# Kernel optimization log

Hardware: AMD Instinct MI355X
Metric: run time of the kernel (lower is better)

The kernel has to match this reference:

```python
import jax, jax.numpy as jnp
import numpy as np

B, D, H = 131072, 8, 128


def setup_inputs() -> dict:
    key = jax.random.key(0)
    ks = jax.random.split(key, 8)
    s1 = 1.0 / np.sqrt(D + 1)
    s2 = 1.0 / np.sqrt(H)
    return {
        "z": jax.random.normal(ks[0], (B, D), dtype=jnp.float32),
        "logp_z": jnp.zeros((B, 1), dtype=jnp.float32),
        "t": jax.random.uniform(ks[1], (1,), dtype=jnp.float32),
        "W1": jax.random.normal(ks[2], (D + 1, H), dtype=jnp.float32) * s1,
        "b1": jnp.zeros((H,), dtype=jnp.float32),
        "W2": jax.random.normal(ks[3], (H, H), dtype=jnp.float32) * s2,
        "b2": jnp.zeros((H,), dtype=jnp.float32),
        "W3": jax.random.normal(ks[4], (H, D), dtype=jnp.float32) * s2,
        "b3": jnp.zeros((D,), dtype=jnp.float32),
    }


def _net_single(z_i, t_scalar, W1, b1, W2, b2, W3, b3):
    # z_i: [D] -> dz/dt: [D]; FFJORD-style MLP on concat([z, t])
    x = jnp.concatenate([z_i, t_scalar[None]])  # [D+1]
    h = jnp.tanh(x @ W1 + b1)
    h = jnp.tanh(h @ W2 + b2)
    return h @ W3 + b3


def reference(z, logp_z, t, W1, b1, W2, b2, W3, b3):
    t_scalar = t.reshape(())

    def f_i(z_i):
        return _net_single(z_i, t_scalar, W1, b1, W2, b2, W3, b3)

    # dz/dt for every sample (batched forward)
    dz_dt = jax.vmap(f_i)(z)  # [B, D]
    # Exact Jacobian trace: fused forward-mode batched Jacobian (replaces the
    # original's D sequential autograd.grad reverse-mode calls)
    jac = jax.vmap(jax.jacfwd(f_i))(z)  # [B, D, D]
    trace = jnp.einsum("bii->b", jac)  # [B]
    dlogp_z_dt = -trace[:, None]  # [B, 1]
    return (dz_dt, dlogp_z_dt)
```

## Files before the change

### kernel.cpp

```cpp
#include <hip/hip_runtime.h>
#include <hip/hip_bf16.h>

#define BATCH 131072
#define PITCH 136

typedef __bf16 bf16x8 __attribute__((ext_vector_type(8)));
typedef float floatx4 __attribute__((ext_vector_type(4)));

__device__ __forceinline__ float fast_tanh(float x) {
    float e = __expf(2.0f * x);
    return 1.0f - 2.0f * __builtin_amdgcn_rcpf(e + 1.0f);
}


__global__ void prep_kernel(const float* __restrict__ W1,
                            const float* __restrict__ W2,
                            const float* __restrict__ W3,
                            __bf16* __restrict__ ws) {
    int idx = blockIdx.x * 256 + threadIdx.x;
    if (idx < 16384) {
        int j = idx & 7, q = (idx >> 3) & 3, n = (idx >> 5) & 127, kb = idx >> 12;
        int k = kb * 32 + q * 8 + j;
        ws[idx] = (__bf16)W2[k * 128 + n];
        float c = 0.0f;
        #pragma unroll
        for (int d = 0; d < 8; ++d) c += W3[k * 8 + d] * W1[d * 128 + n];
        ws[16384 + idx] = (__bf16)(W2[n * 128 + k] * c);
    } else if (idx < 20480) {
        int t = idx - 16384;
        int j = t & 7, q = (t >> 3) & 3, n = t >> 5;
        int k = q * 8 + j;
        ws[32768 + t] = (k < 9) ? (__bf16)W1[k * 128 + n] : (__bf16)0.0f;
    } else if (idx < 22528) {
        int t = idx - 20480;
        int j = t & 7, q = (t >> 3) & 3, n = (t >> 5) & 15, kb = t >> 9;
        int k = kb * 32 + q * 8 + j;
        ws[36864 + t] = (n < 8) ? (__bf16)W3[k * 8 + n] : (__bf16)0.0f;
    }
}

__global__ __launch_bounds__(256, 2) void cnf_main(
        const float* __restrict__ z, const float* __restrict__ t_ptr,
        const float* __restrict__ b1g, const float* __restrict__ b2g,
        const float* __restrict__ b3g, const __bf16* __restrict__ ws,
        float* __restrict__ out) {
    __shared__ __bf16 sW2s[16384];
    __shared__ float sb1[128];
    __shared__ float sb2[128];
    __shared__ __bf16 tile[4][16 * PITCH];

    const int tid = threadIdx.x;
    {
        uint4* dst = (uint4*)sW2s;
        const uint4* src = (const uint4*)ws;
        #pragma unroll
        for (int i = 0; i < 8; ++i) dst[tid + i * 256] = src[tid + i * 256];
        if (tid < 128) { sb1[tid] = b1g[tid]; sb2[tid] = b2g[tid]; }
    }
    __syncthreads();

    const int lane = tid & 63;
    const int w = tid >> 6;
    const int p = lane & 15;
    const int q = lane >> 4;
    __bf16* T = tile[w];
    const float tval = t_ptr[0];
    const float b3v = (p < 8) ? b3g[p] : 0.0f;
    const bf16x8* W2sv = (const bf16x8*)sW2s;
    const bf16x8* GTv  = (const bf16x8*)(ws + 16384);
    const bf16x8* W1g  = (const bf16x8*)(ws + 32768);
    const bf16x8* W3v  = (const bf16x8*)(ws + 36864);

    bf16x8 w1f[8];
    #pragma unroll
    for (int nt = 0; nt < 8; ++nt) w1f[nt] = W1g[(nt * 16 + p) * 4 + q];

    #pragma unroll
    for (int it = 0; it < 2; ++it) {
        const int s0 = blockIdx.x * 128 + it * 64 + w * 16;

        bf16x8 ax;
        #pragma unroll
        for (int j = 0; j < 8; ++j) ax[j] = (__bf16)0.0f;
        if (q == 0) {
            const float4 z0 = ((const float4*)(z + (size_t)(s0 + p) * 8))[0];
            const float4 z1 = ((const float4*)(z + (size_t)(s0 + p) * 8))[1];
            ax[0] = (__bf16)z0.x; ax[1] = (__bf16)z0.y;
            ax[2] = (__bf16)z0.z; ax[3] = (__bf16)z0.w;
            ax[4] = (__bf16)z1.x; ax[5] = (__bf16)z1.y;
            ax[6] = (__bf16)z1.z; ax[7] = (__bf16)z1.w;
        } else if (q == 1) {
            ax[0] = (__bf16)tval;
        }

        float a1c[32];
        #pragma unroll
        for (int nt = 0; nt < 8; ++nt) {
            const int n = nt * 16 + p;
            floatx4 acc = {0.f, 0.f, 0.f, 0.f};
            acc = __builtin_amdgcn_mfma_f32_16x16x32_bf16(ax, w1f[nt], acc, 0, 0, 0);
            const float bn = sb1[n];
            #pragma unroll
            for (int r = 0; r < 4; ++r) {
                const float h1 = fast_tanh(acc[r] + bn);
                a1c[nt * 4 + r] = __builtin_fmaf(-h1, h1, 1.0f);
                T[(q * 4 + r) * PITCH + n] = (__bf16)h1;
            }
        }
        bf16x8 ah[4];
        #pragma unroll
        for (int kb = 0; kb < 4; ++kb)
            ah[kb] = *(const bf16x8*)&T[p * PITCH + kb * 32 + q * 8];

        #pragma unroll
        for (int nt = 0; nt < 8; ++nt) {
            const int n = nt * 16 + p;
            floatx4 acc = {0.f, 0.f, 0.f, 0.f};
            #pragma unroll
            for (int kb = 0; kb < 4; ++kb)
                acc = __builtin_amdgcn_mfma_f32_16x16x32_bf16(
                        ah[kb], W2sv[(kb * 128 + n) * 4 + q], acc, 0, 0, 0);
            const float bn = sb2[n];
            #pragma unroll
            for (int r = 0; r < 4; ++r) {
                const float h2 = fast_tanh(acc[r] + bn);
                T[(q * 4 + r) * PITCH + n] = (__bf16)h2;
            }
        }
        bf16x8 ah2[4];
        bf16x8 aa[4];
        #pragma unroll
        for (int kb = 0; kb < 4; ++kb) {
            ah2[kb] = *(const bf16x8*)&T[p * PITCH + kb * 32 + q * 8];
            #pragma unroll
            for (int j = 0; j < 8; ++j) {
                const float f = (float)ah2[kb][j];
                aa[kb][j] = (__bf16)__builtin_fmaf(-f, f, 1.0f);
            }
        }

        floatx4 acc3 = {0.f, 0.f, 0.f, 0.f};
        #pragma unroll
        for (int kb = 0; kb < 4; ++kb)
            acc3 = __builtin_amdgcn_mfma_f32_16x16x32_bf16(
                    ah2[kb], W3v[(kb * 16 + p) * 4 + q], acc3, 0, 0, 0);
        if (p < 8) {
            #pragma unroll
            for (int r = 0; r < 4; ++r)
                out[(size_t)(s0 + q * 4 + r) * 8 + p] = acc3[r] + b3v;
        }

        float tr[4] = {0.f, 0.f, 0.f, 0.f};
        #pragma unroll
        for (int nt = 0; nt < 8; ++nt) {
            const int n = nt * 16 + p;
            floatx4 acc = {0.f, 0.f, 0.f, 0.f};
            #pragma unroll
            for (int kb = 0; kb < 4; ++kb)
                acc = __builtin_amdgcn_mfma_f32_16x16x32_bf16(
                        aa[kb], GTv[(kb * 128 + n) * 4 + q], acc, 0, 0, 0);
            #pragma unroll
            for (int r = 0; r < 4; ++r)
                tr[r] = __builtin_fmaf(a1c[nt * 4 + r], acc[r], tr[r]);
        }

        #pragma unroll
        for (int r = 0; r < 4; ++r) {
            float v = tr[r];
            v += __shfl_xor(v, 1, 64);
            v += __shfl_xor(v, 2, 64);
            v += __shfl_xor(v, 4, 64);
            v += __shfl_xor(v, 8, 64);
            tr[r] = v;
        }
        if (p == 0) {
            #pragma unroll
            for (int r = 0; r < 4; ++r)
                out[(size_t)BATCH * 8 + s0 + q * 4 + r] = -tr[r];
        }
    }
}

extern "C" void kernel_launch(void* const* d_in, const int* in_sizes, int n_in,
                              void* d_out, int out_size, void* d_ws, size_t ws_size,
                              hipStream_t stream) {
    const float* z  = (const float*)d_in[0];
    const float* t  = (const float*)d_in[2];
    const float* W1 = (const float*)d_in[3];
    const float* b1 = (const float*)d_in[4];
    const float* W2 = (const float*)d_in[5];
    const float* b2 = (const float*)d_in[6];
    const float* W3 = (const float*)d_in[7];
    const float* b3 = (const float*)d_in[8];
    __bf16* ws = (__bf16*)d_ws;
    float* out = (float*)d_out;

    prep_kernel<<<88, 256, 0, stream>>>(W1, W2, W3, ws);
    cnf_main<<<1024, 256, 0, stream>>>(z, t, b1, b2, b3, ws, out);
}
```

Measured before the change: 105.6 us.

## Stage GT matrix in LDS, preload W3 fragments, halve transpose tile

Copies the 32 KB GT matrix (W2 scaled by W3·W1) into shared memory per block instead of reading it from global/L2 inside the trace GEMM loop. W3 fragments are preloaded into registers once. The per-wave transpose tile is cut to half width and filled and read back in two halves, so the extra LDS fits. LDS per block roughly doubles, which may limit the intended two blocks per CU and adds a larger prologue copy for each of the 1024 blocks.

```diff
diff --git a/kernel.cpp b/kernel.cpp
--- a/kernel.cpp
+++ b/kernel.cpp
@@ -2,7 +2,7 @@
 #include <hip/hip_bf16.h>
 
 #define BATCH 131072
-#define PITCH 136
+#define PITCH_H 72
 
 typedef __bf16 bf16x8 __attribute__((ext_vector_type(8)));
 typedef float floatx4 __attribute__((ext_vector_type(4)));
@@ -45,9 +45,10 @@
         const float* __restrict__ b3g, const __bf16* __restrict__ ws,
         float* __restrict__ out) {
     __shared__ __bf16 sW2s[16384];
+    __shared__ __bf16 sGTs[16384];
     __shared__ float sb1[128];
     __shared__ float sb2[128];
-    __shared__ __bf16 tile[4][16 * PITCH];
+    __shared__ __bf16 tile[4][16 * PITCH_H];
 
     const int tid = threadIdx.x;
     {
@@ -55,6 +56,10 @@
         const uint4* src = (const uint4*)ws;
         #pragma unroll
         for (int i = 0; i < 8; ++i) dst[tid + i * 256] = src[tid + i * 256];
+        uint4* dstg = (uint4*)sGTs;
+        const uint4* srcg = (const uint4*)(ws + 16384);
+        #pragma unroll
+        for (int i = 0; i < 8; ++i) dstg[tid + i * 256] = srcg[tid + i * 256];
         if (tid < 128) { sb1[tid] = b1g[tid]; sb2[tid] = b2g[tid]; }
     }
     __syncthreads();
@@ -67,13 +72,16 @@
     const float tval = t_ptr[0];
     const float b3v = (p < 8) ? b3g[p] : 0.0f;
     const bf16x8* W2sv = (const bf16x8*)sW2s;
-    const bf16x8* GTv  = (const bf16x8*)(ws + 16384);
+    const bf16x8* GTsv = (const bf16x8*)sGTs;
     const bf16x8* W1g  = (const bf16x8*)(ws + 32768);
-    const bf16x8* W3v  = (const bf16x8*)(ws + 36864);
+    const bf16x8* W3g  = (const bf16x8*)(ws + 36864);
 
     bf16x8 w1f[8];
     #pragma unroll
     for (int nt = 0; nt < 8; ++nt) w1f[nt] = W1g[(nt * 16 + p) * 4 + q];
+    bf16x8 w3f[4];
+    #pragma unroll
+    for (int kb = 0; kb < 4; ++kb) w3f[kb] = W3g[(kb * 16 + p) * 4 + q];
 
     #pragma unroll
     for (int it = 0; it < 2; ++it) {
@@ -94,44 +102,51 @@
         }
 
         float a1c[32];
-        #pragma unroll
-        for (int nt = 0; nt < 8; ++nt) {
-            const int n = nt * 16 + p;
-            floatx4 acc = {0.f, 0.f, 0.f, 0.f};
-            acc = __builtin_amdgcn_mfma_f32_16x16x32_bf16(ax, w1f[nt], acc, 0, 0, 0);
-            const float bn = sb1[n];
-            #pragma unroll
-            for (int r = 0; r < 4; ++r) {
-                const float h1 = fast_tanh(acc[r] + bn);
-                a1c[nt * 4 + r] = __builtin_fmaf(-h1, h1, 1.0f);
-                T[(q * 4 + r) * PITCH + n] = (__bf16)h1;
+        bf16x8 ah[4];
+        #pragma unroll
+        for (int half = 0; half < 2; ++half) {
+            #pragma unroll
+            for (int nt = half * 4; nt < half * 4 + 4; ++nt) {
+                const int n = nt * 16 + p;
+                floatx4 acc = {0.f, 0.f, 0.f, 0.f};
+                acc = __builtin_amdgcn_mfma_f32_16x16x32_bf16(ax, w1f[nt], acc, 0, 0, 0);
+                const float bn = sb1[n];
+                #pragma unroll
+                for (int r = 0; r < 4; ++r) {
+                    const float h1 = fast_tanh(acc[r] + bn);
+                    a1c[nt * 4 + r] = __builtin_fmaf(-h1, h1, 1.0f);
+                    T[(q * 4 + r) * PITCH_H + (nt - half * 4) * 16 + p] = (__bf16)h1;
+                }
             }
-        }
-        bf16x8 ah[4];
-        #pragma unroll
-        for (int kb = 0; kb < 4; ++kb)
-            ah[kb] = *(const bf16x8*)&T[p * PITCH + kb * 32 + q * 8];
-
-        #pragma unroll
-        for (int nt = 0; nt < 8; ++nt) {
-            const int n = nt * 16 + p;
-            floatx4 acc = {0.f, 0.f, 0.f, 0.f};
-            #pragma unroll
-            for (int kb = 0; kb < 4; ++kb)
-                acc = __builtin_amdgcn_mfma_f32_16x16x32_bf16(
-                        ah[kb], W2sv[(kb * 128 + n) * 4 + q], acc, 0, 0, 0);
-            const float bn = sb2[n];
-            #pragma unroll
-            for (int r = 0; r < 4; ++r) {
-                const float h2 = fast_tanh(acc[r] + bn);
-                T[(q * 4 + r) * PITCH + n] = (__bf16)h2;
+            ah[half * 2 + 0] = *(const bf16x8*)&T[p * PITCH_H + q * 8];
+            ah[half * 2 + 1] = *(const bf16x8*)&T[p * PITCH_H + 32 + q * 8];
+        }
+
+        bf16x8 ah2[4];
+        #pragma unroll
+        for (int half = 0; half < 2; ++half) {
+            #pragma unroll
+            for (int nt = half * 4; nt < half * 4 + 4; ++nt) {
+                const int n = nt * 16 + p;
+                floatx4 acc = {0.f, 0.f, 0.f, 0.f};
+                #pragma unroll
+                for (int kb = 0; kb < 4; ++kb)
+                    acc = __builtin_amdgcn_mfma_f32_16x16x32_bf16(
+                            ah[kb], W2sv[(kb * 128 + n) * 4 + q], acc, 0, 0, 0);
+                const float bn = sb2[n];
+                #pragma unroll
+                for (int r = 0; r < 4; ++r) {
+                    const float h2 = fast_tanh(acc[r] + bn);
+                    T[(q * 4 + r) * PITCH_H + (nt - half * 4) * 16 + p] = (__bf16)h2;
+                }
             }
-        }
-        bf16x8 ah2[4];
+            ah2[half * 2 + 0] = *(const bf16x8*)&T[p * PITCH_H + q * 8];
+            ah2[half * 2 + 1] = *(const bf16x8*)&T[p * PITCH_H + 32 + q * 8];
+        }
+
         bf16x8 aa[4];
         #pragma unroll
         for (int kb = 0; kb < 4; ++kb) {
-            ah2[kb] = *(const bf16x8*)&T[p * PITCH + kb * 32 + q * 8];
             #pragma unroll
             for (int j = 0; j < 8; ++j) {
                 const float f = (float)ah2[kb][j];
@@ -143,7 +158,7 @@
         #pragma unroll
         for (int kb = 0; kb < 4; ++kb)
             acc3 = __builtin_amdgcn_mfma_f32_16x16x32_bf16(
-                    ah2[kb], W3v[(kb * 16 + p) * 4 + q], acc3, 0, 0, 0);
+                    ah2[kb], w3f[kb], acc3, 0, 0, 0);
         if (p < 8) {
             #pragma unroll
             for (int r = 0; r < 4; ++r)
@@ -158,7 +173,7 @@
             #pragma unroll
             for (int kb = 0; kb < 4; ++kb)
                 acc = __builtin_amdgcn_mfma_f32_16x16x32_bf16(
-                        aa[kb], GTv[(kb * 128 + n) * 4 + q], acc, 0, 0, 0);
+                        aa[kb], GTsv[(kb * 128 + n) * 4 + q], acc, 0, 0, 0);
             #pragma unroll
             for (int r = 0; r < 4; ++r)
                 tr[r] = __builtin_fmaf(a1c[nt * 4 + r], acc[r], tr[r]);
```

New measurement: 96.31 us. 1.1x faster.
